# Optimization experiments

Hardware: AMD Instinct MI355X
Metric: run time of the kernel (lower is better)

## Reference

```python
import jax, jax.numpy as jnp
import numpy as np

D_MODEL = 768
NHEAD = 12
WINDOW = 128
FREQ = 10000.0


def _rope(x, freq=FREQ):
    # x: (b, h, l, d). Rotate-half style rotary embedding.
    b, h, l, d = x.shape
    inv_freq = 1.0 / (freq ** (jnp.arange(0, d, 2, dtype=jnp.float32) / d))  # (d/2,)
    ang = jnp.arange(l, dtype=jnp.float32)[:, None] * inv_freq[None, :]      # (l, d/2)
    cos = jnp.cos(ang)[None, None]  # (1,1,l,d/2)
    sin = jnp.sin(ang)[None, None]
    x1, x2 = x[..., : d // 2], x[..., d // 2 :]
    return jnp.concatenate([x1 * cos - x2 * sin, x1 * sin + x2 * cos], axis=-1)


def setup_inputs() -> dict:
    key = jax.random.key(0)
    k0, k1, k2 = jax.random.split(key, 3)
    B, L = 1, 2048
    emb = jax.random.normal(k0, (B, L, D_MODEL), dtype=jnp.float32)
    mask = jnp.ones((B, L), dtype=jnp.int32)
    W_qkv = jax.random.normal(k1, (D_MODEL, 3 * D_MODEL), dtype=jnp.float32) * 0.02
    b_qkv = jnp.zeros((3 * D_MODEL,), dtype=jnp.float32)
    W_o = jax.random.normal(k2, (D_MODEL, D_MODEL), dtype=jnp.float32) * 0.02
    b_o = jnp.zeros((D_MODEL,), dtype=jnp.float32)
    return {"embeddings": emb, "attention_mask": mask, "W_qkv": W_qkv, "b_qkv": b_qkv, "W_o": W_o, "b_o": b_o}


def reference(embeddings, attention_mask, W_qkv, b_qkv, W_o, b_o):
    B, L, D = embeddings.shape
    H, W = NHEAD, WINDOW
    hd = D // H
    scale = 1.0 / jnp.sqrt(jnp.float32(D))  # original divides by d_model**0.5

    qkv = embeddings @ W_qkv + b_qkv                      # (b,l,3D)
    q, k, v = jnp.split(qkv, 3, axis=-1)

    def sep(x):  # (b,l,D) -> (b,h,l,hd)
        return x.reshape(B, L, H, hd).transpose(0, 2, 1, 3)

    q, k, v = sep(q), sep(k), sep(v)
    q = _rope(q)
    k = _rope(k)

    # window indices: centered window of width W, clamped to [0, L-1]
    raw = jnp.arange(L)[:, None] + jnp.arange(W)[None, :] - W // 2  # (L,W)
    idxs = jnp.clip(raw, 0, L - 1)
    in_range = (raw >= 0) & (raw < L)                                # (L,W)

    k_w = k[:, :, idxs, :]  # (b,h,l,w,hd) gathered keys
    v_w = v[:, :, idxs, :]

    scores = jnp.einsum("bhlwd,bhld->bhlw", k_w, q) * scale
    amask = attention_mask.astype(bool)                              # (b,l)
    wmask = amask[:, idxs] & in_range[None]                          # (b,l,w)
    scores = jnp.where(wmask[:, None], scores, -jnp.inf)
    weights = jax.nn.softmax(scores, axis=-1)
    out = jnp.einsum("bhlw,bhlwd->bhld", weights, v_w)               # (b,h,l,hd)

    # CLS global attention (query at position 0 attends to all keys)
    cls_scores = jnp.einsum("bhd,bhld->bhl", q[:, :, 0, :], k) * scale
    cls_scores = jnp.where(amask[:, None], cls_scores, -jnp.inf)
    cls_w = jax.nn.softmax(cls_scores, axis=-1)
    cls_out = jnp.einsum("bhl,bhld->bhd", cls_w, v)                  # (b,h,hd)
    out = out.at[:, :, 0, :].set(cls_out)

    joined = out.transpose(0, 2, 1, 3).reshape(B, L, D)              # join heads
    return joined @ W_o + b_o
```

## Files before the change

kernel.cpp:

```cpp
#include <hip/hip_runtime.h>
#include <hip/hip_bf16.h>
#include <cmath>

#define D_MODEL 768
#define NHEAD 12
#define HD 64
#define L_SEQ 2048
#define WIN 128
#define QKV_N (3 * D_MODEL)

typedef _Float16 half8 __attribute__((ext_vector_type(8)));
typedef _Float16 half4v __attribute__((ext_vector_type(4)));
typedef float floatx4 __attribute__((ext_vector_type(4)));

__global__ __launch_bounds__(256) void cvt16_kernel(const float* __restrict__ In,
                                                    _Float16* __restrict__ Out,
                                                    int n) {
  const int i = (blockIdx.x * 256 + threadIdx.x) * 4;
  if (i < n) {
    const float4 v = *reinterpret_cast<const float4*>(&In[i]);
    half4v h = {(_Float16)v.x, (_Float16)v.y, (_Float16)v.z, (_Float16)v.w};
    *reinterpret_cast<half4v*>(&Out[i]) = h;
  }
}

__global__ __launch_bounds__(256) void cvt_transpose16_kernel(
    const float* __restrict__ In, _Float16* __restrict__ Out, int R, int Cn) {
  __shared__ float tile[64][68];
  const int tid = threadIdx.x;
  const int r0 = blockIdx.y * 64;
  const int c0 = blockIdx.x * 64;
  const int tr = tid >> 4;
  const int tc4 = (tid & 15) * 4;
#pragma unroll
  for (int rr = 0; rr < 4; ++rr) {
    const int r = rr * 16 + tr;
    const float4 v =
        *reinterpret_cast<const float4*>(&In[(size_t)(r0 + r) * Cn + c0 + tc4]);
    tile[r][tc4 + 0] = v.x;
    tile[r][tc4 + 1] = v.y;
    tile[r][tc4 + 2] = v.z;
    tile[r][tc4 + 3] = v.w;
  }
  __syncthreads();
#pragma unroll
  for (int cc = 0; cc < 4; ++cc) {
    const int c = cc * 16 + tr;
    half4v h = {(_Float16)tile[tc4 + 0][c], (_Float16)tile[tc4 + 1][c],
                (_Float16)tile[tc4 + 2][c], (_Float16)tile[tc4 + 3][c]};
    *reinterpret_cast<half4v*>(&Out[(size_t)(c0 + c) * R + r0 + tc4]) = h;
  }
}

template <int BM, int BN, typename OutT, bool ROPE>
__global__ __launch_bounds__(256) void gemm16_kernel(
    const _Float16* __restrict__ A, const _Float16* __restrict__ BT,
    const float* __restrict__ bias, OutT* __restrict__ C,
    _Float16* __restrict__ q16, _Float16* __restrict__ k16,
    _Float16* __restrict__ v16, int M, int N, int K) {
  constexpr int LDK = 40;
  constexpr int MF = BM / 32;
  constexpr int NF = BN / 32;
  constexpr int CA = BM * 4 / 256;
  constexpr int CB = BN * 4 / 256;

  __shared__ __align__(16) _Float16 At[BM * LDK];
  __shared__ __align__(16) _Float16 Bt[BN * LDK];

  const int tid = threadIdx.x;
  const int row0 = blockIdx.y * BM;
  const int col0 = blockIdx.x * BN;
  const int wv = tid >> 6;
  const int lane = tid & 63;
  const int wr = wv >> 1;
  const int wc = wv & 1;
  const int lrow = lane & 15;
  const int lk = lane >> 4;

  floatx4 acc[MF][NF];
#pragma unroll
  for (int m = 0; m < MF; ++m)
#pragma unroll
    for (int n = 0; n < NF; ++n) acc[m][n] = (floatx4){0.f, 0.f, 0.f, 0.f};

  half8 aR[CA], bR[CB];
  const int nt = K / 32;

#pragma unroll
  for (int i = 0; i < CA; ++i) {
    const int c = tid + i * 256, r = c >> 2, seg = c & 3;
    aR[i] = *reinterpret_cast<const half8*>(&A[(size_t)(row0 + r) * K + seg * 8]);
  }
#pragma unroll
  for (int i = 0; i < CB; ++i) {
    const int c = tid + i * 256, r = c >> 2, seg = c & 3;
    bR[i] =
        *reinterpret_cast<const half8*>(&BT[(size_t)(col0 + r) * K + seg * 8]);
  }

  for (int t = 0; t < nt; ++t) {
    if (t) __syncthreads();
#pragma unroll
    for (int i = 0; i < CA; ++i) {
      const int c = tid + i * 256, r = c >> 2, seg = c & 3;
      *reinterpret_cast<half8*>(&At[r * LDK + seg * 8]) = aR[i];
    }
#pragma unroll
    for (int i = 0; i < CB; ++i) {
      const int c = tid + i * 256, r = c >> 2, seg = c & 3;
      *reinterpret_cast<half8*>(&Bt[r * LDK + seg * 8]) = bR[i];
    }
    __syncthreads();

    if (t + 1 < nt) {
      const int k0 = (t + 1) * 32;
#pragma unroll
      for (int i = 0; i < CA; ++i) {
        const int c = tid + i * 256, r = c >> 2, seg = c & 3;
        aR[i] = *reinterpret_cast<const half8*>(
            &A[(size_t)(row0 + r) * K + k0 + seg * 8]);
      }
#pragma unroll
      for (int i = 0; i < CB; ++i) {
        const int c = tid + i * 256, r = c >> 2, seg = c & 3;
        bR[i] = *reinterpret_cast<const half8*>(
            &BT[(size_t)(col0 + r) * K + k0 + seg * 8]);
      }
    }

    half8 af[MF], bf[NF];
#pragma unroll
    for (int m = 0; m < MF; ++m)
      af[m] = *reinterpret_cast<const half8*>(
          &At[(wr * (BM / 2) + m * 16 + lrow) * LDK + lk * 8]);
#pragma unroll
    for (int n = 0; n < NF; ++n)
      bf[n] = *reinterpret_cast<const half8*>(
          &Bt[(wc * (BN / 2) + n * 16 + lrow) * LDK + lk * 8]);
#pragma unroll
    for (int m = 0; m < MF; ++m)
#pragma unroll
      for (int n = 0; n < NF; ++n)
        acc[m][n] = __builtin_amdgcn_mfma_f32_16x16x32_f16(af[m], bf[n],
                                                           acc[m][n], 0, 0, 0);
  }

  if constexpr (!ROPE) {
#pragma unroll
    for (int m = 0; m < MF; ++m)
#pragma unroll
      for (int n = 0; n < NF; ++n) {
        const int col = col0 + wc * (BN / 2) + n * 16 + lrow;
        const float bb = bias[col];
#pragma unroll
        for (int j = 0; j < 4; ++j) {
          const int row = row0 + wr * (BM / 2) + m * 16 + lk * 4 + j;
          C[(size_t)row * N + col] = (OutT)(acc[m][n][j] + bb);
        }
      }
  } else {
    const int part = col0 / D_MODEL;
    const int h = ((col0 % D_MODEL) >> 6) + wc;
    _Float16* dst = (part == 0) ? q16 : (part == 1) ? k16 : v16;
    float bb[4];
#pragma unroll
    for (int n = 0; n < 4; ++n) bb[n] = bias[col0 + wc * 64 + n * 16 + lrow];
    const float inv0 = exp2f(-0.4152410118609203f * (float)lrow);
    const float inv1 = inv0 * 0.01f;
#pragma unroll
    for (int m = 0; m < MF; ++m)
#pragma unroll
      for (int j = 0; j < 4; ++j) {
        const int l = row0 + wr * (BM / 2) + m * 16 + lk * 4 + j;
        float val[4];
#pragma unroll
        for (int n = 0; n < 4; ++n) val[n] = acc[m][n][j] + bb[n];
        float o[4];
        if (part < 2) {
          float sn0, cs0, sn1, cs1;
          __sincosf((float)l * inv0, &sn0, &cs0);
          __sincosf((float)l * inv1, &sn1, &cs1);
          o[0] = val[0] * cs0 - val[2] * sn0;
          o[1] = val[1] * cs1 - val[3] * sn1;
          o[2] = val[0] * sn0 + val[2] * cs0;
          o[3] = val[1] * sn1 + val[3] * cs1;
        } else {
          o[0] = val[0]; o[1] = val[1]; o[2] = val[2]; o[3] = val[3];
        }
        const size_t base = ((size_t)h * L_SEQ + l) * HD + lrow;
#pragma unroll
        for (int n = 0; n < 4; ++n) dst[base + n * 16] = (_Float16)o[n];
      }
  }
}

#define TL 32
#define SLOTS 160
#define LDH 72
#define LDS_S 168
#define LDVT 168

__global__ __launch_bounds__(256) void win_attn_kernel(
    const _Float16* __restrict__ q16, const _Float16* __restrict__ k16,
    const _Float16* __restrict__ v16, const int* __restrict__ mask,
    _Float16* __restrict__ joined) {
  const int l0 = blockIdx.x * TL;
  const int h = blockIdx.y;
  const int tid = threadIdx.x;
  const float scale = 0.036084391824351615f;

  __shared__ __align__(16) _Float16 kv16[SLOTS * LDH];
  __shared__ __align__(16) float sS[TL * LDS_S];
  __shared__ __align__(16) _Float16 q16l[TL * LDH];
  __shared__ float vbias[SLOTS];

  const _Float16* kh = k16 + (size_t)h * L_SEQ * HD;
  const _Float16* vh = v16 + (size_t)h * L_SEQ * HD;
  const _Float16* qh = q16 + (size_t)h * L_SEQ * HD;

  {
    const int row = tid >> 3, oct = (tid & 7) * 8;
    *reinterpret_cast<half8*>(&q16l[row * LDH + oct]) =
        *reinterpret_cast<const half8*>(&qh[(size_t)(l0 + row) * HD + oct]);
  }
#pragma unroll
  for (int c = tid; c < SLOTS * 8; c += 256) {
    const int slot = c >> 3, oct = (c & 7) * 8;
    const int raw = l0 + slot - WIN / 2;
    const int idx = min(max(raw, 0), L_SEQ - 1);
    *reinterpret_cast<half8*>(&kv16[slot * LDH + oct]) =
        *reinterpret_cast<const half8*>(&kh[(size_t)idx * HD + oct]);
  }
  if (tid < SLOTS) {
    const int raw = l0 + tid - WIN / 2;
    const int idx = min(max(raw, 0), L_SEQ - 1);
    vbias[tid] =
        ((raw >= 0) && (raw < L_SEQ) && (mask[idx] != 0)) ? 0.f : -INFINITY;
  }
  __syncthreads();

  const int wv = tid >> 6, lane = tid & 63;
  const int wr = wv >> 1, wc = wv & 1;
  const int lcol = lane & 15, loct = (lane >> 4) * 8;

  floatx4 accS[5];
#pragma unroll
  for (int f = 0; f < 5; ++f) accS[f] = (floatx4){0.f, 0.f, 0.f, 0.f};
#pragma unroll
  for (int ks = 0; ks < 2; ++ks) {
    const half8 af = *reinterpret_cast<const half8*>(
        &q16l[(wr * 16 + lcol) * LDH + ks * 32 + loct]);
#pragma unroll
    for (int f = 0; f < 5; ++f) {
      const half8 bf = *reinterpret_cast<const half8*>(
          &kv16[(wc * 80 + f * 16 + lcol) * LDH + ks * 32 + loct]);
      accS[f] =
          __builtin_amdgcn_mfma_f32_16x16x32_f16(af, bf, accS[f], 0, 0, 0);
    }
  }
#pragma unroll
  for (int f = 0; f < 5; ++f) {
    const int slot = wc * 80 + f * 16 + lcol;
    const float vb = vbias[slot];
#pragma unroll
    for (int j = 0; j < 4; ++j) {
      const int row = wr * 16 + (lane >> 4) * 4 + j;
      const bool inband = (slot >= row) && (slot <= row + WIN - 1);
      sS[row * LDS_S + slot] = inband ? (accS[f][j] * scale + vb) : -INFINITY;
    }
  }
  __syncthreads();

  _Float16* vt = kv16;
#pragma unroll
  for (int c = tid; c < SLOTS * 8; c += 256) {
    const int slot = c >> 3, d0 = (c & 7) * 8;
    const int raw = l0 + slot - WIN / 2;
    const int idx = min(max(raw, 0), L_SEQ - 1);
    const half8 vv =
        *reinterpret_cast<const half8*>(&vh[(size_t)idx * HD + d0]);
#pragma unroll
    for (int e = 0; e < 8; ++e) vt[(d0 + e) * LDVT + slot] = vv[e];
  }

  const int r = tid >> 3, wg = tid & 7;
  float pv[20];
  float mloc = -INFINITY;
#pragma unroll
  for (int i = 0; i < 20; ++i) {
    pv[i] = sS[r * LDS_S + wg * 20 + i];
    mloc = fmaxf(mloc, pv[i]);
  }
#pragma unroll
  for (int m = 1; m < 8; m <<= 1) mloc = fmaxf(mloc, __shfl_xor(mloc, m));
  float ssum = 0.f;
#pragma unroll
  for (int i = 0; i < 20; ++i) {
    pv[i] = __expf(pv[i] - mloc);
    ssum += pv[i];
  }
#pragma unroll
  for (int m = 1; m < 8; m <<= 1) ssum += __shfl_xor(ssum, m);
  const float rcp = 1.0f / ssum;
  __syncthreads();

  _Float16* pS = reinterpret_cast<_Float16*>(sS);
#pragma unroll
  for (int i = 0; i < 20; ++i)
    pS[r * (2 * LDS_S) + wg * 20 + i] = (_Float16)(pv[i] * rcp);
  __syncthreads();

  floatx4 accO[2];
  accO[0] = (floatx4){0.f, 0.f, 0.f, 0.f};
  accO[1] = (floatx4){0.f, 0.f, 0.f, 0.f};
#pragma unroll
  for (int ks = 0; ks < 5; ++ks) {
    const half8 ap = *reinterpret_cast<const half8*>(
        &pS[(wr * 16 + lcol) * (2 * LDS_S) + ks * 32 + loct]);
#pragma unroll
    for (int cf = 0; cf < 2; ++cf) {
      const half8 bv = *reinterpret_cast<const half8*>(
          &vt[(wc * 32 + cf * 16 + lcol) * LDVT + ks * 32 + loct]);
      accO[cf] =
          __builtin_amdgcn_mfma_f32_16x16x32_f16(ap, bv, accO[cf], 0, 0, 0);
    }
  }
#pragma unroll
  for (int cf = 0; cf < 2; ++cf)
#pragma unroll
    for (int j = 0; j < 4; ++j) {
      const int row = wr * 16 + (lane >> 4) * 4 + j;
      const int d = wc * 32 + cf * 16 + lcol;
      joined[(size_t)(l0 + row) * D_MODEL + h * HD + d] =
          (_Float16)accO[cf][j];
    }
}

#define CSPLIT 32
#define CROWS (L_SEQ / CSPLIT)
#define CREC 66

__global__ __launch_bounds__(256) void cls_partial_kernel(
    const _Float16* __restrict__ q16, const _Float16* __restrict__ k16,
    const _Float16* __restrict__ v16, const int* __restrict__ mask,
    float* __restrict__ part) {
  const int h = blockIdx.x;
  const int sp = blockIdx.y;
  const int tid = threadIdx.x;
  const int l0 = sp * CROWS;
  const float scale = 0.036084391824351615f;

  __shared__ float scS[CROWS];
  __shared__ float red[256];
  __shared__ float pvS[4][HD];

  const _Float16* kh = k16 + (size_t)h * L_SEQ * HD;
  const _Float16* vh = v16 + (size_t)h * L_SEQ * HD;

  const int lq = tid >> 4;
  const int dq = tid & 15;
  const half4v q4 =
      *reinterpret_cast<const half4v*>(&q16[(size_t)h * L_SEQ * HD + dq * 4]);
#pragma unroll
  for (int it = 0; it < CROWS / 16; ++it) {
    const int l = l0 + it * 16 + lq;
    const half4v k4 =
        *reinterpret_cast<const half4v*>(&kh[(size_t)l * HD + dq * 4]);
    float p = (float)q4[0] * (float)k4[0] + (float)q4[1] * (float)k4[1] +
              (float)q4[2] * (float)k4[2] + (float)q4[3] * (float)k4[3];
#pragma unroll
    for (int m = 1; m < 16; m <<= 1) p += __shfl_xor(p, m);
    if (dq == 0) scS[it * 16 + lq] = (mask[l] != 0) ? p * scale : -INFINITY;
  }
  __syncthreads();

  red[tid] = (tid < CROWS) ? scS[tid] : -INFINITY;
  __syncthreads();
  for (int off = 128; off > 0; off >>= 1) {
    if (tid < off) red[tid] = fmaxf(red[tid], red[tid + off]);
    __syncthreads();
  }
  const float mx = red[0];
  __syncthreads();

  float e = 0.f;
  if (tid < CROWS) {
    e = (mx == -INFINITY) ? 0.f : __expf(scS[tid] - mx);
    scS[tid] = e;
  }
  red[tid] = e;
  __syncthreads();
  for (int off = 128; off > 0; off >>= 1) {
    if (tid < off) red[tid] += red[tid + off];
    __syncthreads();
  }
  const float lsum = red[0];
  __syncthreads();

  const int lg = tid >> 6;
  const int d = tid & 63;
  float acc = 0.f;
#pragma unroll 8
  for (int it = 0; it < CROWS / 4; ++it) {
    const int ll = lg + it * 4;
    acc += scS[ll] * (float)vh[(size_t)(l0 + ll) * HD + d];
  }
  pvS[lg][d] = acc;
  __syncthreads();

  float* rec = &part[(size_t)(h * CSPLIT + sp) * CREC];
  if (tid == 0) {
    rec[0] = mx;
    rec[1] = lsum;
  }
  if (tid < HD)
    rec[2 + tid] = pvS[0][tid] + pvS[1][tid] + pvS[2][tid] + pvS[3][tid];
}

__global__ __launch_bounds__(64) void cls_combine_kernel(
    const float* __restrict__ part, _Float16* __restrict__ joined) {
  const int h = blockIdx.x;
  const int d = threadIdx.x;

  float gmax = -INFINITY;
#pragma unroll
  for (int sp = 0; sp < CSPLIT; ++sp)
    gmax = fmaxf(gmax, part[(size_t)(h * CSPLIT + sp) * CREC]);

  float total = 0.f, acc = 0.f;
#pragma unroll
  for (int sp = 0; sp < CSPLIT; ++sp) {
    const float* rec = &part[(size_t)(h * CSPLIT + sp) * CREC];
    const float mxi = rec[0];
    const float w = (mxi == -INFINITY) ? 0.f : __expf(mxi - gmax);
    total += w * rec[1];
    acc += w * rec[2 + d];
  }
  joined[(size_t)h * HD + d] = (_Float16)(acc / total);
}

extern "C" void kernel_launch(void* const* d_in, const int* in_sizes, int n_in,
                              void* d_out, int out_size, void* d_ws,
                              size_t ws_size, hipStream_t stream) {
  const float* emb   = (const float*)d_in[0];
  const int*   mask  = (const int*)d_in[1];
  const float* W_qkv = (const float*)d_in[2];
  const float* b_qkv = (const float*)d_in[3];
  const float* W_o   = (const float*)d_in[4];
  const float* b_o   = (const float*)d_in[5];
  float* out = (float*)d_out;

  _Float16* hp = (_Float16*)d_ws;
  _Float16* A16   = hp;
  _Float16* Wq16T = A16 + (size_t)L_SEQ * D_MODEL;
  _Float16* Wo16T = Wq16T + (size_t)QKV_N * D_MODEL;
  _Float16* q16   = Wo16T + (size_t)D_MODEL * D_MODEL;
  _Float16* k16   = q16 + (size_t)NHEAD * L_SEQ * HD;
  _Float16* v16   = k16 + (size_t)NHEAD * L_SEQ * HD;
  _Float16* J16   = v16 + (size_t)NHEAD * L_SEQ * HD;
  float*    part  = (float*)(J16 + (size_t)L_SEQ * D_MODEL);

  cvt16_kernel<<<(L_SEQ * D_MODEL) / 1024, 256, 0, stream>>>(
      emb, A16, L_SEQ * D_MODEL);
  cvt_transpose16_kernel<<<dim3(QKV_N / 64, D_MODEL / 64), 256, 0, stream>>>(
      W_qkv, Wq16T, D_MODEL, QKV_N);
  cvt_transpose16_kernel<<<dim3(D_MODEL / 64, D_MODEL / 64), 256, 0, stream>>>(
      W_o, Wo16T, D_MODEL, D_MODEL);

  gemm16_kernel<64, 128, _Float16, true>
      <<<dim3(QKV_N / 128, L_SEQ / 64), 256, 0, stream>>>(
          A16, Wq16T, b_qkv, (_Float16*)nullptr, q16, k16, v16, L_SEQ, QKV_N,
          D_MODEL);

  cls_partial_kernel<<<dim3(NHEAD, CSPLIT), 256, 0, stream>>>(q16, k16, v16,
                                                              mask, part);

  win_attn_kernel<<<dim3(L_SEQ / TL, NHEAD), 256, 0, stream>>>(q16, k16, v16,
                                                               mask, J16);

  cls_combine_kernel<<<NHEAD, 64, 0, stream>>>(part, J16);

  gemm16_kernel<64, 64, float, false>
      <<<dim3(D_MODEL / 64, L_SEQ / 64), 256, 0, stream>>>(
          J16, Wo16T, b_o, out, (_Float16*)nullptr, (_Float16*)nullptr,
          (_Float16*)nullptr, L_SEQ, D_MODEL, D_MODEL);
}
```

Before: 130.8 us.

## Fuse conversion and attention launches, emit transposed V from the QKV GEMM epilogue

Merges the three fp32-to-fp16 conversion kernels into one launch that dispatches on block index. The QKV GEMM epilogue additionally writes a transposed copy of V, so the window attention can load V rows with vector loads instead of scattering elements into a transposed LDS layout. The CLS partial-attention blocks and the window-attention blocks become one launch, and the K window is loaded without index clamping, relying on the -inf bias for out-of-range slots. This cuts launch count and LDS scatter work at the cost of extra V storage and reads past the head boundary, which depend on the neighbouring memory holding finite values.

```diff
diff --git a/kernel.cpp b/kernel.cpp
--- a/kernel.cpp
+++ b/kernel.cpp
@@ -13,25 +13,39 @@
 typedef _Float16 half4v __attribute__((ext_vector_type(4)));
 typedef float floatx4 __attribute__((ext_vector_type(4)));
 
-__global__ __launch_bounds__(256) void cvt16_kernel(const float* __restrict__ In,
-                                                    _Float16* __restrict__ Out,
-                                                    int n) {
-  const int i = (blockIdx.x * 256 + threadIdx.x) * 4;
-  if (i < n) {
-    const float4 v = *reinterpret_cast<const float4*>(&In[i]);
+#define CVT_A_BLKS 1536
+#define CVT_B_BLKS (36 * 12)
+#define CVT_C_BLKS (12 * 12)
+
+__global__ __launch_bounds__(256) void cvt_fused_kernel(
+    const float* __restrict__ emb, _Float16* __restrict__ A16,
+    const float* __restrict__ W_qkv, _Float16* __restrict__ Wq16T,
+    const float* __restrict__ W_o, _Float16* __restrict__ Wo16T) {
+  __shared__ float tile[64][68];
+  const int bid = blockIdx.x;
+  const int tid = threadIdx.x;
+
+  if (bid < CVT_A_BLKS) {
+    const int i = (bid * 256 + tid) * 4;
+    const float4 v = *reinterpret_cast<const float4*>(&emb[i]);
     half4v h = {(_Float16)v.x, (_Float16)v.y, (_Float16)v.z, (_Float16)v.w};
-    *reinterpret_cast<half4v*>(&Out[i]) = h;
-  }
-}
-
-__global__ __launch_bounds__(256) void cvt_transpose16_kernel(
-    const float* __restrict__ In, _Float16* __restrict__ Out, int R, int Cn) {
-  __shared__ float tile[64][68];
-  const int tid = threadIdx.x;
-  const int r0 = blockIdx.y * 64;
-  const int c0 = blockIdx.x * 64;
-  const int tr = tid >> 4;
-  const int tc4 = (tid & 15) * 4;
+    *reinterpret_cast<half4v*>(&A16[i]) = h;
+    return;
+  }
+  const float* In;
+  _Float16* Out;
+  int R, Cn, bx, by;
+  if (bid < CVT_A_BLKS + CVT_B_BLKS) {
+    const int b = bid - CVT_A_BLKS;
+    In = W_qkv; Out = Wq16T; R = D_MODEL; Cn = QKV_N;
+    bx = b % 36; by = b / 36;
+  } else {
+    const int b = bid - CVT_A_BLKS - CVT_B_BLKS;
+    In = W_o; Out = Wo16T; R = D_MODEL; Cn = D_MODEL;
+    bx = b % 12; by = b / 12;
+  }
+  const int r0 = by * 64, c0 = bx * 64;
+  const int tr = tid >> 4, tc4 = (tid & 15) * 4;
 #pragma unroll
   for (int rr = 0; rr < 4; ++rr) {
     const int r = rr * 16 + tr;
@@ -57,7 +71,8 @@
     const _Float16* __restrict__ A, const _Float16* __restrict__ BT,
     const float* __restrict__ bias, OutT* __restrict__ C,
     _Float16* __restrict__ q16, _Float16* __restrict__ k16,
-    _Float16* __restrict__ v16, int M, int N, int K) {
+    _Float16* __restrict__ v16, _Float16* __restrict__ v16T, int M, int N,
+    int K) {
   constexpr int LDK = 40;
   constexpr int MF = BM / 32;
   constexpr int NF = BN / 32;
@@ -168,7 +183,7 @@
     const float inv0 = exp2f(-0.4152410118609203f * (float)lrow);
     const float inv1 = inv0 * 0.01f;
 #pragma unroll
-    for (int m = 0; m < MF; ++m)
+    for (int m = 0; m < MF; ++m) {
 #pragma unroll
       for (int j = 0; j < 4; ++j) {
         const int l = row0 + wr * (BM / 2) + m * 16 + lk * 4 + j;
@@ -191,6 +206,19 @@
 #pragma unroll
         for (int n = 0; n < 4; ++n) dst[base + n * 16] = (_Float16)o[n];
       }
+      if (part == 2) {
+        const int lb = row0 + wr * (BM / 2) + m * 16 + lk * 4;
+#pragma unroll
+        for (int n = 0; n < 4; ++n) {
+          const int col = h * HD + n * 16 + lrow;
+          half4v hv = {(_Float16)(acc[m][n][0] + bb[n]),
+                       (_Float16)(acc[m][n][1] + bb[n]),
+                       (_Float16)(acc[m][n][2] + bb[n]),
+                       (_Float16)(acc[m][n][3] + bb[n])};
+          *reinterpret_cast<half4v*>(&v16T[(size_t)col * L_SEQ + lb]) = hv;
+        }
+      }
+    }
   }
 }
 
@@ -199,12 +227,15 @@
 #define LDH 72
 #define LDS_S 168
 #define LDVT 168
-
-__global__ __launch_bounds__(256) void win_attn_kernel(
+#define CSPLIT 32
+#define CROWS (L_SEQ / CSPLIT)
+#define CREC 66
+
+__global__ __launch_bounds__(256) void attn_mega_kernel(
     const _Float16* __restrict__ q16, const _Float16* __restrict__ k16,
-    const _Float16* __restrict__ v16, const int* __restrict__ mask,
-    _Float16* __restrict__ joined) {
-  const int l0 = blockIdx.x * TL;
+    const _Float16* __restrict__ v16, const _Float16* __restrict__ v16T,
+    const int* __restrict__ mask, _Float16* __restrict__ joined,
+    float* __restrict__ part) {
   const int h = blockIdx.y;
   const int tid = threadIdx.x;
   const float scale = 0.036084391824351615f;
@@ -214,207 +245,195 @@
   __shared__ __align__(16) _Float16 q16l[TL * LDH];
   __shared__ float vbias[SLOTS];
 
-  const _Float16* kh = k16 + (size_t)h * L_SEQ * HD;
-  const _Float16* vh = v16 + (size_t)h * L_SEQ * HD;
-  const _Float16* qh = q16 + (size_t)h * L_SEQ * HD;
-
-  {
-    const int row = tid >> 3, oct = (tid & 7) * 8;
-    *reinterpret_cast<half8*>(&q16l[row * LDH + oct]) =
-        *reinterpret_cast<const half8*>(&qh[(size_t)(l0 + row) * HD + oct]);
-  }
-#pragma unroll
-  for (int c = tid; c < SLOTS * 8; c += 256) {
-    const int slot = c >> 3, oct = (c & 7) * 8;
-    const int raw = l0 + slot - WIN / 2;
-    const int idx = min(max(raw, 0), L_SEQ - 1);
-    *reinterpret_cast<half8*>(&kv16[slot * LDH + oct]) =
-        *reinterpret_cast<const half8*>(&kh[(size_t)idx * HD + oct]);
-  }
-  if (tid < SLOTS) {
-    const int raw = l0 + tid - WIN / 2;
-    const int idx = min(max(raw, 0), L_SEQ - 1);
-    vbias[tid] =
-        ((raw >= 0) && (raw < L_SEQ) && (mask[idx] != 0)) ? 0.f : -INFINITY;
-  }
-  __syncthreads();
-
-  const int wv = tid >> 6, lane = tid & 63;
-  const int wr = wv >> 1, wc = wv & 1;
-  const int lcol = lane & 15, loct = (lane >> 4) * 8;
-
-  floatx4 accS[5];
-#pragma unroll
-  for (int f = 0; f < 5; ++f) accS[f] = (floatx4){0.f, 0.f, 0.f, 0.f};
-#pragma unroll
-  for (int ks = 0; ks < 2; ++ks) {
-    const half8 af = *reinterpret_cast<const half8*>(
-        &q16l[(wr * 16 + lcol) * LDH + ks * 32 + loct]);
+  if (blockIdx.x < (L_SEQ / TL)) {
+    const int l0 = blockIdx.x * TL;
+    const _Float16* kh = k16 + (size_t)h * L_SEQ * HD;
+    const _Float16* qh = q16 + (size_t)h * L_SEQ * HD;
+
+    {
+      const int row = tid >> 3, oct = (tid & 7) * 8;
+      *reinterpret_cast<half8*>(&q16l[row * LDH + oct]) =
+          *reinterpret_cast<const half8*>(&qh[(size_t)(l0 + row) * HD + oct]);
+    }
+    const _Float16* kwin = kh + (size_t)(l0 - WIN / 2) * HD;
+#pragma unroll
+    for (int c = tid; c < SLOTS * 8; c += 256) {
+      const int slot = c >> 3, oct = (c & 7) * 8;
+      *reinterpret_cast<half8*>(&kv16[slot * LDH + oct]) =
+          *reinterpret_cast<const half8*>(&kwin[(size_t)slot * HD + oct]);
+    }
+    if (tid < SLOTS) {
+      const int raw = l0 + tid - WIN / 2;
+      const int idx = min(max(raw, 0), L_SEQ - 1);
+      vbias[tid] =
+          ((raw >= 0) && (raw < L_SEQ) && (mask[idx] != 0)) ? 0.f : -INFINITY;
+    }
+    __syncthreads();
+
+    const int wv = tid >> 6, lane = tid & 63;
+    const int wr = wv >> 1, wc = wv & 1;
+    const int lcol = lane & 15, loct = (lane >> 4) * 8;
+
+    floatx4 accS[5];
+#pragma unroll
+    for (int f = 0; f < 5; ++f) accS[f] = (floatx4){0.f, 0.f, 0.f, 0.f};
+#pragma unroll
+    for (int ks = 0; ks < 2; ++ks) {
+      const half8 af = *reinterpret_cast<const half8*>(
+          &q16l[(wr * 16 + lcol) * LDH + ks * 32 + loct]);
+#pragma unroll
+      for (int f = 0; f < 5; ++f) {
+        const half8 bf = *reinterpret_cast<const half8*>(
+            &kv16[(wc * 80 + f * 16 + lcol) * LDH + ks * 32 + loct]);
+        accS[f] =
+            __builtin_amdgcn_mfma_f32_16x16x32_f16(af, bf, accS[f], 0, 0, 0);
+      }
+    }
 #pragma unroll
     for (int f = 0; f < 5; ++f) {
-      const half8 bf = *reinterpret_cast<const half8*>(
-          &kv16[(wc * 80 + f * 16 + lcol) * LDH + ks * 32 + loct]);
-      accS[f] =
-          __builtin_amdgcn_mfma_f32_16x16x32_f16(af, bf, accS[f], 0, 0, 0);
-    }
-  }
-#pragma unroll
-  for (int f = 0; f < 5; ++f) {
-    const int slot = wc * 80 + f * 16 + lcol;
-    const float vb = vbias[slot];
-#pragma unroll
-    for (int j = 0; j < 4; ++j) {
-      const int row = wr * 16 + (lane >> 4) * 4 + j;
-      const bool inband = (slot >= row) && (slot <= row + WIN - 1);
-      sS[row * LDS_S + slot] = inband ? (accS[f][j] * scale + vb) : -INFINITY;
-    }
-  }
-  __syncthreads();
-
-  _Float16* vt = kv16;
-#pragma unroll
-  for (int c = tid; c < SLOTS * 8; c += 256) {
-    const int slot = c >> 3, d0 = (c & 7) * 8;
-    const int raw = l0 + slot - WIN / 2;
-    const int idx = min(max(raw, 0), L_SEQ - 1);
-    const half8 vv =
-        *reinterpret_cast<const half8*>(&vh[(size_t)idx * HD + d0]);
-#pragma unroll
-    for (int e = 0; e < 8; ++e) vt[(d0 + e) * LDVT + slot] = vv[e];
-  }
-
-  const int r = tid >> 3, wg = tid & 7;
-  float pv[20];
-  float mloc = -INFINITY;
-#pragma unroll
-  for (int i = 0; i < 20; ++i) {
-    pv[i] = sS[r * LDS_S + wg * 20 + i];
-    mloc = fmaxf(mloc, pv[i]);
-  }
-#pragma unroll
-  for (int m = 1; m < 8; m <<= 1) mloc = fmaxf(mloc, __shfl_xor(mloc, m));
-  float ssum = 0.f;
-#pragma unroll
-  for (int i = 0; i < 20; ++i) {
-    pv[i] = __expf(pv[i] - mloc);
-    ssum += pv[i];
-  }
-#pragma unroll
-  for (int m = 1; m < 8; m <<= 1) ssum += __shfl_xor(ssum, m);
-  const float rcp = 1.0f / ssum;
-  __syncthreads();
-
-  _Float16* pS = reinterpret_cast<_Float16*>(sS);
-#pragma unroll
-  for (int i = 0; i < 20; ++i)
-    pS[r * (2 * LDS_S) + wg * 20 + i] = (_Float16)(pv[i] * rcp);
-  __syncthreads();
-
-  floatx4 accO[2];
-  accO[0] = (floatx4){0.f, 0.f, 0.f, 0.f};
-  accO[1] = (floatx4){0.f, 0.f, 0.f, 0.f};
-#pragma unroll
-  for (int ks = 0; ks < 5; ++ks) {
-    const half8 ap = *reinterpret_cast<const half8*>(
-        &pS[(wr * 16 + lcol) * (2 * LDS_S) + ks * 32 + loct]);
-#pragma unroll
-    for (int cf = 0; cf < 2; ++cf) {
-      const half8 bv = *reinterpret_cast<const half8*>(
-          &vt[(wc * 32 + cf * 16 + lcol) * LDVT + ks * 32 + loct]);
-      accO[cf] =
-          __builtin_amdgcn_mfma_f32_16x16x32_f16(ap, bv, accO[cf], 0, 0, 0);
-    }
-  }
-#pragma unroll
-  for (int cf = 0; cf < 2; ++cf)
-#pragma unroll
-    for (int j = 0; j < 4; ++j) {
-      const int row = wr * 16 + (lane >> 4) * 4 + j;
-      const int d = wc * 32 + cf * 16 + lcol;
-      joined[(size_t)(l0 + row) * D_MODEL + h * HD + d] =
-          (_Float16)accO[cf][j];
-    }
-}
-
-#define CSPLIT 32
-#define CROWS (L_SEQ / CSPLIT)
-#define CREC 66
-
-__global__ __launch_bounds__(256) void cls_partial_kernel(
-    const _Float16* __restrict__ q16, const _Float16* __restrict__ k16,
-    const _Float16* __restrict__ v16, const int* __restrict__ mask,
-    float* __restrict__ part) {
-  const int h = blockIdx.x;
-  const int sp = blockIdx.y;
-  const int tid = threadIdx.x;
-  const int l0 = sp * CROWS;
-  const float scale = 0.036084391824351615f;
-
-  __shared__ float scS[CROWS];
-  __shared__ float red[256];
-  __shared__ float pvS[4][HD];
-
-  const _Float16* kh = k16 + (size_t)h * L_SEQ * HD;
-  const _Float16* vh = v16 + (size_t)h * L_SEQ * HD;
-
-  const int lq = tid >> 4;
-  const int dq = tid & 15;
-  const half4v q4 =
-      *reinterpret_cast<const half4v*>(&q16[(size_t)h * L_SEQ * HD + dq * 4]);
-#pragma unroll
-  for (int it = 0; it < CROWS / 16; ++it) {
-    const int l = l0 + it * 16 + lq;
-    const half4v k4 =
-        *reinterpret_cast<const half4v*>(&kh[(size_t)l * HD + dq * 4]);
-    float p = (float)q4[0] * (float)k4[0] + (float)q4[1] * (float)k4[1] +
-              (float)q4[2] * (float)k4[2] + (float)q4[3] * (float)k4[3];
-#pragma unroll
-    for (int m = 1; m < 16; m <<= 1) p += __shfl_xor(p, m);
-    if (dq == 0) scS[it * 16 + lq] = (mask[l] != 0) ? p * scale : -INFINITY;
-  }
-  __syncthreads();
-
-  red[tid] = (tid < CROWS) ? scS[tid] : -INFINITY;
-  __syncthreads();
-  for (int off = 128; off > 0; off >>= 1) {
-    if (tid < off) red[tid] = fmaxf(red[tid], red[tid + off]);
-    __syncthreads();
-  }
-  const float mx = red[0];
-  __syncthreads();
-
-  float e = 0.f;
-  if (tid < CROWS) {
-    e = (mx == -INFINITY) ? 0.f : __expf(scS[tid] - mx);
-    scS[tid] = e;
-  }
-  red[tid] = e;
-  __syncthreads();
-  for (int off = 128; off > 0; off >>= 1) {
-    if (tid < off) red[tid] += red[tid + off];
-    __syncthreads();
-  }
-  const float lsum = red[0];
-  __syncthreads();
-
-  const int lg = tid >> 6;
-  const int d = tid & 63;
-  float acc = 0.f;
+      const int slot = wc * 80 + f * 16 + lcol;
+      const float vb = vbias[slot];
+#pragma unroll
+      for (int j = 0; j < 4; ++j) {
+        const int row = wr * 16 + (lane >> 4) * 4 + j;
+        const bool inband = (slot >= row) && (slot <= row + WIN - 1);
+        sS[row * LDS_S + slot] = inband ? (accS[f][j] * scale + vb) : -INFINITY;
+      }
+    }
+    __syncthreads();
+
+    _Float16* vt = kv16;
+    const _Float16* vtg =
+        v16T + (size_t)h * HD * L_SEQ + (l0 - WIN / 2);
+#pragma unroll
+    for (int c = tid; c < HD * 20; c += 256) {
+      const int d = c / 20, seg = c % 20;
+      *reinterpret_cast<half8*>(&vt[d * LDVT + seg * 8]) =
+          *reinterpret_cast<const half8*>(&vtg[(size_t)d * L_SEQ + seg * 8]);
+    }
+
+    const int r = tid >> 3, wg = tid & 7;
+    float pv[20];
+    float mloc = -INFINITY;
+#pragma unroll
+    for (int i = 0; i < 20; ++i) {
+      pv[i] = sS[r * LDS_S + wg * 20 + i];
+      mloc = fmaxf(mloc, pv[i]);
+    }
+#pragma unroll
+    for (int m = 1; m < 8; m <<= 1) mloc = fmaxf(mloc, __shfl_xor(mloc, m));
+    float ssum = 0.f;
+#pragma unroll
+    for (int i = 0; i < 20; ++i) {
+      pv[i] = __expf(pv[i] - mloc);
+      ssum += pv[i];
+    }
+#pragma unroll
+    for (int m = 1; m < 8; m <<= 1) ssum += __shfl_xor(ssum, m);
+    const float rcp = 1.0f / ssum;
+    __syncthreads();
+
+    _Float16* pS = reinterpret_cast<_Float16*>(sS);
+#pragma unroll
+    for (int i = 0; i < 20; ++i)
+      pS[r * (2 * LDS_S) + wg * 20 + i] = (_Float16)(pv[i] * rcp);
+    __syncthreads();
+
+    floatx4 accO[2];
+    accO[0] = (floatx4){0.f, 0.f, 0.f, 0.f};
+    accO[1] = (floatx4){0.f, 0.f, 0.f, 0.f};
+#pragma unroll
+    for (int ks = 0; ks < 5; ++ks) {
+      const half8 ap = *reinterpret_cast<const half8*>(
+          &pS[(wr * 16 + lcol) * (2 * LDS_S) + ks * 32 + loct]);
+#pragma unroll
+      for (int cf = 0; cf < 2; ++cf) {
+        const half8 bv = *reinterpret_cast<const half8*>(
+            &vt[(wc * 32 + cf * 16 + lcol) * LDVT + ks * 32 + loct]);
+        accO[cf] =
+            __builtin_amdgcn_mfma_f32_16x16x32_f16(ap, bv, accO[cf], 0, 0, 0);
+      }
+    }
+#pragma unroll
+    for (int cf = 0; cf < 2; ++cf)
+#pragma unroll
+      for (int j = 0; j < 4; ++j) {
+        const int row = wr * 16 + (lane >> 4) * 4 + j;
+        const int d = wc * 32 + cf * 16 + lcol;
+        joined[(size_t)(l0 + row) * D_MODEL + h * HD + d] =
+            (_Float16)accO[cf][j];
+      }
+  } else {
+    const int sp = blockIdx.x - (L_SEQ / TL);
+    const int l0 = sp * CROWS;
+    float* scS = sS;
+    float* red = sS + CROWS;
+    float* pvS = sS + CROWS + 256;
+
+    const _Float16* kh = k16 + (size_t)h * L_SEQ * HD;
+    const _Float16* vh = v16 + (size_t)h * L_SEQ * HD;
+
+    const int lq = tid >> 4;
+    const int dq = tid & 15;
+    const half4v q4 =
+        *reinterpret_cast<const half4v*>(&q16[(size_t)h * L_SEQ * HD + dq * 4]);
+#pragma unroll
+    for (int it = 0; it < CROWS / 16; ++it) {
+      const int l = l0 + it * 16 + lq;
+      const half4v k4 =
+          *reinterpret_cast<const half4v*>(&kh[(size_t)l * HD + dq * 4]);
+      float p = (float)q4[0] * (float)k4[0] + (float)q4[1] * (float)k4[1] +
+                (float)q4[2] * (float)k4[2] + (float)q4[3] * (float)k4[3];
+#pragma unroll
+      for (int m = 1; m < 16; m <<= 1) p += __shfl_xor(p, m);
+      if (dq == 0) scS[it * 16 + lq] = (mask[l] != 0) ? p * scale : -INFINITY;
+    }
+    __syncthreads();
+
+    red[tid] = (tid < CROWS) ? scS[tid] : -INFINITY;
+    __syncthreads();
+    for (int off = 128; off > 0; off >>= 1) {
+      if (tid < off) red[tid] = fmaxf(red[tid], red[tid + off]);
+      __syncthreads();
+    }
+    const float mx = red[0];
+    __syncthreads();
+
+    float e = 0.f;
+    if (tid < CROWS) {
+      e = (mx == -INFINITY) ? 0.f : __expf(scS[tid] - mx);
+      scS[tid] = e;
+    }
+    red[tid] = e;
+    __syncthreads();
+    for (int off = 128; off > 0; off >>= 1) {
+      if (tid < off) red[tid] += red[tid + off];
+      __syncthreads();
+    }
+    const float lsum = red[0];
+    __syncthreads();
+
+    const int lg = tid >> 6;
+    const int d = tid & 63;
+    float acc = 0.f;
 #pragma unroll 8
-  for (int it = 0; it < CROWS / 4; ++it) {
-    const int ll = lg + it * 4;
-    acc += scS[ll] * (float)vh[(size_t)(l0 + ll) * HD + d];
-  }
-  pvS[lg][d] = acc;
-  __syncthreads();
-
-  float* rec = &part[(size_t)(h * CSPLIT + sp) * CREC];
-  if (tid == 0) {
-    rec[0] = mx;
-    rec[1] = lsum;
-  }
-  if (tid < HD)
-    rec[2 + tid] = pvS[0][tid] + pvS[1][tid] + pvS[2][tid] + pvS[3][tid];
+    for (int it = 0; it < CROWS / 4; ++it) {
+      const int ll = lg + it * 4;
+      acc += scS[ll] * (float)vh[(size_t)(l0 + ll) * HD + d];
+    }
+    pvS[lg * HD + d] = acc;
+    __syncthreads();
+
+    float* rec = &part[(size_t)(h * CSPLIT + sp) * CREC];
+    if (tid == 0) {
+      rec[0] = mx;
+      rec[1] = lsum;
+    }
+    if (tid < HD)
+      rec[2 + tid] =
+          pvS[0 * HD + tid] + pvS[1 * HD + tid] + pvS[2 * HD + tid] +
+          pvS[3 * HD + tid];
+  }
 }
 
 __global__ __launch_bounds__(64) void cls_combine_kernel(
@@ -457,31 +476,25 @@
   _Float16* q16   = Wo16T + (size_t)D_MODEL * D_MODEL;
   _Float16* k16   = q16 + (size_t)NHEAD * L_SEQ * HD;
   _Float16* v16   = k16 + (size_t)NHEAD * L_SEQ * HD;
-  _Float16* J16   = v16 + (size_t)NHEAD * L_SEQ * HD;
+  _Float16* v16T  = v16 + (size_t)NHEAD * L_SEQ * HD;
+  _Float16* J16   = v16T + (size_t)D_MODEL * L_SEQ;
   float*    part  = (float*)(J16 + (size_t)L_SEQ * D_MODEL);
 
-  cvt16_kernel<<<(L_SEQ * D_MODEL) / 1024, 256, 0, stream>>>(
-      emb, A16, L_SEQ * D_MODEL);
-  cvt_transpose16_kernel<<<dim3(QKV_N / 64, D_MODEL / 64), 256, 0, stream>>>(
-      W_qkv, Wq16T, D_MODEL, QKV_N);
-  cvt_transpose16_kernel<<<dim3(D_MODEL / 64, D_MODEL / 64), 256, 0, stream>>>(
-      W_o, Wo16T, D_MODEL, D_MODEL);
+  cvt_fused_kernel<<<CVT_A_BLKS + CVT_B_BLKS + CVT_C_BLKS, 256, 0, stream>>>(
+      emb, A16, W_qkv, Wq16T, W_o, Wo16T);
 
   gemm16_kernel<64, 128, _Float16, true>
       <<<dim3(QKV_N / 128, L_SEQ / 64), 256, 0, stream>>>(
-          A16, Wq16T, b_qkv, (_Float16*)nullptr, q16, k16, v16, L_SEQ, QKV_N,
-          D_MODEL);
-
-  cls_partial_kernel<<<dim3(NHEAD, CSPLIT), 256, 0, stream>>>(q16, k16, v16,
-                                                              mask, part);
-
-  win_attn_kernel<<<dim3(L_SEQ / TL, NHEAD), 256, 0, stream>>>(q16, k16, v16,
-                                                               mask, J16);
+          A16, Wq16T, b_qkv, (_Float16*)nullptr, q16, k16, v16, v16T, L_SEQ,
+          QKV_N, D_MODEL);
+
+  attn_mega_kernel<<<dim3(L_SEQ / TL + CSPLIT, NHEAD), 256, 0, stream>>>(
+      q16, k16, v16, v16T, mask, J16, part);
 
   cls_combine_kernel<<<NHEAD, 64, 0, stream>>>(part, J16);
 
   gemm16_kernel<64, 64, float, false>
       <<<dim3(D_MODEL / 64, L_SEQ / 64), 256, 0, stream>>>(
           J16, Wo16T, b_o, out, (_Float16*)nullptr, (_Float16*)nullptr,
-          (_Float16*)nullptr, L_SEQ, D_MODEL, D_MODEL);
+          (_Float16*)nullptr, (_Float16*)nullptr, L_SEQ, D_MODEL, D_MODEL);
 }
```

New measurement: 123.8 us. -5.3%, faster.
